# Kernel tuning notes

Measured on AMD Instinct MI355X. Metric: run time of the kernel, lower is better.

Reference implementation:

```python
import jax, jax.numpy as jnp
import numpy as np

DIM = 768
HEADS = 12
DIM_HEAD = DIM // HEADS
FACTOR = DIM_HEAD ** (-0.5)
B, T = 4, 2048


def setup_inputs() -> dict:
    key = jax.random.key(0)
    k1, k2, k3 = jax.random.split(key, 3)
    x = jax.random.normal(k1, (B, T, DIM), dtype=jnp.float32)
    # VarianceScaling-like init scale for linear weights
    W_qkv = jax.random.normal(k2, (DIM, 3 * DIM), dtype=jnp.float32) * (DIM ** -0.5)
    W_out = jax.random.normal(k3, (DIM, DIM), dtype=jnp.float32) * (DIM ** -0.5)
    return {"x": x, "W_qkv": W_qkv, "W_out": W_out}


def reference(x, W_qkv, W_out):
    b, t, _ = x.shape
    qkv = x @ W_qkv  # [b, t, 3*dim]
    # einops 'b t (d k h) -> k b h t d' with k=3, h=HEADS: d slowest, k middle, h fastest
    qkv = qkv.reshape(b, t, DIM_HEAD, 3, HEADS)
    qkv = jnp.transpose(qkv, (3, 0, 4, 1, 2))  # [3, b, h, t, d]
    q, k, v = qkv[0], qkv[1], qkv[2]
    # scaled dot-product attention, full [b,h,t,t] scores as in the original
    scores = jnp.einsum('bhid,bhjd->bhij', q, k) * FACTOR
    attn = jax.nn.softmax(scores, axis=-1)
    out = jnp.einsum('bhij,bhjd->bhid', attn, v)  # [b, h, t, d]
    # 'b h t d -> b t (h d)'
    out = jnp.transpose(out, (0, 2, 1, 3)).reshape(b, t, HEADS * DIM_HEAD)
    return out @ W_out
```

## Files before the change

kernel.cpp:

```cpp
#include <hip/hip_runtime.h>
#include <hip/hip_bf16.h>

#define DIM    768
#define HEADS  12
#define DHEAD  64
#define BATCH  4
#define SEQ    2048
#define NROW   (BATCH * SEQ)
#define QKVN   (3 * DIM)
#define FACTOR 0.125f
#define QSCALE 0.18033688011112042f

typedef __attribute__((ext_vector_type(8))) short short8;
typedef __attribute__((ext_vector_type(4))) float floatx4;

__device__ __forceinline__ floatx4 mfma16(short8 a, short8 b, floatx4 c) {
    return __builtin_amdgcn_mfma_f32_16x16x32_bf16(a, b, c, 0, 0, 0);
}

__device__ __forceinline__ void glds16(const void* g, void* l) {
    __builtin_amdgcn_global_load_lds((const __attribute__((address_space(1))) void*)g,
                                     (__attribute__((address_space(3))) void*)l,
                                     16, 0, 0);
}

__device__ __forceinline__ short rne16(float f) {
    unsigned u = __builtin_bit_cast(unsigned, f);
    return (short)((u + 0x7fffu + ((u >> 16) & 1u)) >> 16);
}
__device__ __forceinline__ unsigned pack2(float lo, float hi) {
    unsigned ul = __builtin_bit_cast(unsigned, lo);
    unsigned uh = __builtin_bit_cast(unsigned, hi);
    ul = (ul + 0x7fffu + ((ul >> 16) & 1u)) >> 16;
    uh = (uh + 0x7fffu + ((uh >> 16) & 1u)) & 0xffff0000u;
    return ul | uh;
}

__device__ __forceinline__ int swz8(int row, int col) {
    return (row << 6) + ((((col >> 3) ^ row) & 7) << 3) + (col & 7);
}

__global__ __launch_bounds__(256) void prep(const float* __restrict__ x,
                                            short* __restrict__ xb,
                                            const float* __restrict__ Wqkv,
                                            short* __restrict__ Wqt,
                                            const float* __restrict__ Wout,
                                            short* __restrict__ Wot) {
    __shared__ short T[32][33];
    int blk = blockIdx.x;
    if (blk < 6144) {
        int g = blk * 256 + threadIdx.x;
        float4 v = ((const float4*)x)[g];
        uint2 o;
        o.x = pack2(v.x, v.y);
        o.y = pack2(v.z, v.w);
        ((uint2*)xb)[g] = o;
        return;
    }
    blk -= 6144;
    const float* W;
    short* Wt;
    int N, permute, bx, by;
    if (blk < 1728) { W = Wqkv; Wt = Wqt; N = QKVN; permute = 1; bx = blk % 72; by = blk / 72; }
    else { blk -= 1728; W = Wout; Wt = Wot; N = DIM; permute = 0; bx = blk % 24; by = blk / 24; }

    int n0 = bx * 32, k0 = by * 32;
    int c = threadIdx.x & 31, r0 = threadIdx.x >> 5;
    for (int r = r0; r < 32; r += 8)
        T[r][c] = rne16(W[(size_t)(k0 + r) * N + n0 + c]);
    __syncthreads();
    for (int r = r0; r < 32; r += 8) {
        int n = n0 + r;
        int np = n;
        float scale = 1.0f;
        if (permute) {
            int d = n / 36, rem = n - d * 36;
            int which = rem / 12, h = rem - which * 12;
            np = which * 768 + h * 64 + d;
            if (which == 0) scale = QSCALE;
        }
        float v = __bfloat162float(__hip_bfloat16_raw{(unsigned short)T[c][r]});
        Wt[(size_t)np * DIM + k0 + c] = (scale == 1.0f) ? T[c][r] : rne16(v * scale);
    }
}

__global__ __launch_bounds__(256) void gemm_qkv(const short* __restrict__ A,
                                                const short* __restrict__ Bt,
                                                short* __restrict__ Qo,
                                                short* __restrict__ Ko,
                                                short* __restrict__ Vto) {
    __shared__ short As[128 * 64];
    __shared__ short Bs[128 * 64];
    const int tid = threadIdx.x;
    const int lane = tid & 63, wave = tid >> 6;
    const int l15 = lane & 15, quad = lane >> 4;

    const int flat = blockIdx.x;
    const int xcd = flat & 7;
    const int local = flat >> 3;
    const int mloc = local & 7, nloc = local >> 3;
    const int m0 = (xcd * 8 + mloc) * 128;
    const int n0 = nloc * 128;

    const int wm = (wave >> 1) * 64, wn = (wave & 1) * 64;
    const int r8 = wave * 8 + (lane >> 3);
    const int c8 = lane & 7;
    const int sc = ((c8 ^ (r8 & 7)) << 3);

    const int sn = n0 + wn;
    const int which = sn / 768;
    const bool swapAB = (which != 2);

    floatx4 acc[4][4] = {};
    for (int k0 = 0; k0 < DIM; k0 += 64) {
#pragma unroll
        for (int i = 0; i < 4; ++i) {
            int row = i * 32 + r8;
            glds16(&A[(size_t)(m0 + row) * DIM + k0 + sc], &As[(size_t)(i * 32 + wave * 8) * 64]);
            glds16(&Bt[(size_t)(n0 + row) * DIM + k0 + sc], &Bs[(size_t)(i * 32 + wave * 8) * 64]);
        }
        __syncthreads();
#pragma unroll
        for (int ks = 0; ks < 2; ++ks) {
            short8 a[4], b[4];
#pragma unroll
            for (int mt = 0; mt < 4; ++mt)
                a[mt] = *(const short8*)&As[swz8(wm + mt * 16 + l15, ks * 32 + quad * 8)];
#pragma unroll
            for (int nt = 0; nt < 4; ++nt)
                b[nt] = *(const short8*)&Bs[swz8(wn + nt * 16 + l15, ks * 32 + quad * 8)];
            if (swapAB) {
#pragma unroll
                for (int mt = 0; mt < 4; ++mt)
#pragma unroll
                    for (int nt = 0; nt < 4; ++nt)
                        acc[mt][nt] = mfma16(b[nt], a[mt], acc[mt][nt]);
            } else {
#pragma unroll
                for (int mt = 0; mt < 4; ++mt)
#pragma unroll
                    for (int nt = 0; nt < 4; ++nt)
                        acc[mt][nt] = mfma16(a[mt], b[nt], acc[mt][nt]);
            }
        }
        __syncthreads();
    }

    const int h = (sn - which * 768) >> 6;
    const int bb = (m0 + wm) >> 11;
    const int tbase = (m0 + wm) & 2047;
    const size_t tilebase = ((size_t)(bb * HEADS + h) * 32 + (tbase >> 6)) * 4096;

    if (which != 2) {
        short* dst = (which == 0) ? Qo : Ko;
#pragma unroll
        for (int mt = 0; mt < 4; ++mt)
#pragma unroll
            for (int nt = 0; nt < 4; ++nt) {
                int tl = mt * 16 + l15;
                int d0 = nt * 16 + quad * 4;
                uint2 pk;
                pk.x = pack2(acc[mt][nt][0], acc[mt][nt][1]);
                pk.y = pack2(acc[mt][nt][2], acc[mt][nt][3]);
                *(uint2*)&dst[tilebase + swz8(tl, d0)] = pk;
            }
    } else {
        short* vld = ((wave < 2) ? As : Bs) + (wave & 1) * 4096;
#pragma unroll
        for (int mt = 0; mt < 4; ++mt)
#pragma unroll
            for (int nt = 0; nt < 4; ++nt) {
                int d = nt * 16 + l15;
                int tl = mt * 16 + quad * 4;
                int chunk = (tl >> 3) ^ (d & 7);
                int addr = (d << 6) + (chunk << 3) + (tl & 7);
                uint2 pk;
                pk.x = pack2(acc[mt][nt][0], acc[mt][nt][1]);
                pk.y = pack2(acc[mt][nt][2], acc[mt][nt][3]);
                *(uint2*)&vld[addr] = pk;
            }
    }
    __syncthreads();
    if (which == 2) {
        short* vld = ((wave < 2) ? As : Bs) + (wave & 1) * 4096;
#pragma unroll
        for (int i = 0; i < 8; ++i) {
            int c = (i * 64 + lane) * 8;
            *(uint4*)&Vto[tilebase + c] = *(const uint4*)&vld[c];
        }
    }
}

__global__ __launch_bounds__(512, 6) void attn_mfma(const short* __restrict__ Q,
                                                    const short* __restrict__ K,
                                                    const short* __restrict__ Vt,
                                                    short* __restrict__ O) {
    __shared__ __align__(16) short buf[8192];
    __shared__ __align__(16) short Ps[8192];
    __shared__ float Lx[256];

    const int tid = threadIdx.x;
    const int lane = tid & 63, wave = tid >> 6;
    const int l15 = lane & 15, quad = lane >> 4;
    const int pair = wave >> 1, sh = wave & 1;
    const int flat = blockIdx.x;
    const int xcd = flat & 7, li = flat >> 3;
    const int bh = xcd + (li % 6) * 8;
    const int q0 = (li / 6) * 128;
    const size_t base = (size_t)bh * SEQ * DHEAD;
    short* Ks = buf;
    short* Vs = buf + 4096;
    short* Pp = Ps + pair * 2048;
    const int lane8 = lane * 8;

    {
        size_t qtb = base + (size_t)(q0 >> 6) * 4096;
#pragma unroll
        for (int i = 0; i < 2; ++i)
            glds16(&Q[qtb + (size_t)(i * 8 + wave) * 512 + lane8],
                   &buf[(i * 8 + wave) * 512]);
    }
    __syncthreads();
    short8 qf[2][2];
#pragma unroll
    for (int mt = 0; mt < 2; ++mt)
#pragma unroll
        for (int ks = 0; ks < 2; ++ks)
            qf[mt][ks] = *(const short8*)&buf[swz8(pair * 32 + mt * 16 + l15,
                                                   ks * 32 + quad * 8)];
    __syncthreads();

    floatx4 o[2][2] = {};
    float lsum[2] = {0.f, 0.f};

    for (int j0 = 0; j0 < SEQ; j0 += 64) {
        size_t ktb = base + (size_t)(j0 >> 6) * 4096 + wave * 512 + lane8;
        glds16(&K[ktb], &Ks[wave * 512]);
        glds16(&Vt[ktb], &Vs[wave * 512]);
        __syncthreads();

        floatx4 sa[2][2] = {};
#pragma unroll
        for (int ks = 0; ks < 2; ++ks) {
            short8 kf0 = *(const short8*)&Ks[swz8(sh * 32 + l15, ks * 32 + quad * 8)];
            short8 kf1 = *(const short8*)&Ks[swz8(sh * 32 + 16 + l15, ks * 32 + quad * 8)];
            sa[0][0] = mfma16(kf0, qf[0][ks], sa[0][0]);
            sa[0][1] = mfma16(kf1, qf[0][ks], sa[0][1]);
            sa[1][0] = mfma16(kf0, qf[1][ks], sa[1][0]);
            sa[1][1] = mfma16(kf1, qf[1][ks], sa[1][1]);
        }

#pragma unroll
        for (int mt = 0; mt < 2; ++mt)
#pragma unroll
            for (int kt = 0; kt < 2; ++kt) {
                float p0 = __builtin_amdgcn_exp2f(sa[mt][kt][0]);
                float p1 = __builtin_amdgcn_exp2f(sa[mt][kt][1]);
                float p2 = __builtin_amdgcn_exp2f(sa[mt][kt][2]);
                float p3 = __builtin_amdgcn_exp2f(sa[mt][kt][3]);
                lsum[mt] += (p0 + p1) + (p2 + p3);
                uint2 pk;
                pk.x = pack2(p0, p1);
                pk.y = pack2(p2, p3);
                *(uint2*)&Pp[swz8(mt * 16 + l15, sh * 32 + kt * 16 + quad * 4)] = pk;
            }
        __syncthreads();

#pragma unroll
        for (int ks = 0; ks < 2; ++ks) {
            short8 a0 = *(const short8*)&Pp[swz8(l15, ks * 32 + quad * 8)];
            short8 a1 = *(const short8*)&Pp[swz8(16 + l15, ks * 32 + quad * 8)];
            short8 b0 = *(const short8*)&Vs[swz8(sh * 32 + l15, ks * 32 + quad * 8)];
            short8 b1 = *(const short8*)&Vs[swz8(sh * 32 + 16 + l15, ks * 32 + quad * 8)];
            o[0][0] = mfma16(a0, b0, o[0][0]);
            o[0][1] = mfma16(a0, b1, o[0][1]);
            o[1][0] = mfma16(a1, b0, o[1][0]);
            o[1][1] = mfma16(a1, b1, o[1][1]);
        }
        __syncthreads();
    }

    float r0 = lsum[0], r1 = lsum[1];
    r0 += __shfl_xor(r0, 16); r0 += __shfl_xor(r0, 32);
    r1 += __shfl_xor(r1, 16); r1 += __shfl_xor(r1, 32);
    if (quad == 0) {
        Lx[pair * 64 + sh * 32 + l15] = r0;
        Lx[pair * 64 + sh * 32 + 16 + l15] = r1;
    }
    __syncthreads();
    float inv0 = 1.f / (r0 + Lx[pair * 64 + (sh ^ 1) * 32 + l15]);
    float inv1 = 1.f / (r1 + Lx[pair * 64 + (sh ^ 1) * 32 + 16 + l15]);

    const int b = bh / HEADS, h = bh - b * HEADS;
#pragma unroll
    for (int r = 0; r < 4; ++r) {
        float iv0 = __shfl(inv0, quad * 4 + r);
        float iv1 = __shfl(inv1, quad * 4 + r);
#pragma unroll
        for (int mt = 0; mt < 2; ++mt) {
            int t = q0 + pair * 32 + mt * 16 + quad * 4 + r;
            float iv = mt ? iv1 : iv0;
            size_t rowo = ((size_t)(b * SEQ + t)) * DIM + h * DHEAD + sh * 32;
            O[rowo + l15] = rne16(o[mt][0][r] * iv);
            O[rowo + 16 + l15] = rne16(o[mt][1][r] * iv);
        }
    }
}

__global__ __launch_bounds__(256) void gemm_out(const short* __restrict__ A,
                                                const short* __restrict__ Bt,
                                                float* __restrict__ out) {
    __shared__ short As[128 * 64];
    __shared__ short Bs[128 * 64];
    const int tid = threadIdx.x;
    const int lane = tid & 63, wave = tid >> 6;
    const int l15 = lane & 15, quad = lane >> 4;
    const int m0 = blockIdx.y * 128, n0 = blockIdx.x * 128;
    const int wm = (wave >> 1) * 64, wn = (wave & 1) * 64;
    const int r8 = wave * 8 + (lane >> 3);
    const int sc = (((lane & 7) ^ (r8 & 7)) << 3);

    floatx4 acc[4][4] = {};
    for (int k0 = 0; k0 < DIM; k0 += 64) {
#pragma unroll
        for (int i = 0; i < 4; ++i) {
            int row = i * 32 + r8;
            glds16(&A[(size_t)(m0 + row) * DIM + k0 + sc], &As[(size_t)(i * 32 + wave * 8) * 64]);
            glds16(&Bt[(size_t)(n0 + row) * DIM + k0 + sc], &Bs[(size_t)(i * 32 + wave * 8) * 64]);
        }
        __syncthreads();
#pragma unroll
        for (int ks = 0; ks < 2; ++ks) {
            short8 a[4], b[4];
#pragma unroll
            for (int mt = 0; mt < 4; ++mt)
                a[mt] = *(const short8*)&As[swz8(wm + mt * 16 + l15, ks * 32 + quad * 8)];
#pragma unroll
            for (int nt = 0; nt < 4; ++nt)
                b[nt] = *(const short8*)&Bs[swz8(wn + nt * 16 + l15, ks * 32 + quad * 8)];
#pragma unroll
            for (int mt = 0; mt < 4; ++mt)
#pragma unroll
                for (int nt = 0; nt < 4; ++nt)
                    acc[mt][nt] = mfma16(b[nt], a[mt], acc[mt][nt]);
        }
        __syncthreads();
    }

#pragma unroll
    for (int mt = 0; mt < 4; ++mt)
#pragma unroll
        for (int nt = 0; nt < 4; ++nt) {
            int m = m0 + wm + mt * 16 + l15;
            int n = n0 + wn + nt * 16 + quad * 4;
            *(floatx4*)&out[(size_t)m * DIM + n] = acc[mt][nt];
        }
}

extern "C" void kernel_launch(void* const* d_in, const int* in_sizes, int n_in,
                              void* d_out, int out_size, void* d_ws, size_t ws_size,
                              hipStream_t stream) {
    const float* x    = (const float*)d_in[0];
    const float* Wqkv = (const float*)d_in[1];
    const float* Wout = (const float*)d_in[2];
    float* out = (float*)d_out;

    const size_t NE = (size_t)NROW * DIM;
    short* xb  = (short*)d_ws;
    short* Wqt = xb + NE;
    short* Wot = Wqt + (size_t)QKVN * DIM;
    short* Qw  = Wot + (size_t)DIM * DIM;
    short* Kw  = Qw + NE;
    short* Vtw = Kw + NE;

    prep<<<6144 + 1728 + 576, 256, 0, stream>>>(x, xb, Wqkv, Wqt, Wout, Wot);
    gemm_qkv<<<8 * 8 * 18, 256, 0, stream>>>(xb, Wqt, Qw, Kw, Vtw);
    attn_mfma<<<768, 512, 0, stream>>>(Qw, Kw, Vtw, xb);
    gemm_out<<<dim3(DIM / 128, NROW / 128), 256, 0, stream>>>(xb, Wot, out);
}
```

Measured before the change: 218.1 us.

## Restructure attention kernel: one wave per query strip, double-buffered K/V

Rewrites the attention kernel so each of four waves owns 32 full query rows across all 64 keys and head dims. Wave pairs no longer split the work, which removes the per-tile P sync and the cross-wave row-sum exchange. K/V tiles are double-buffered in LDS, so the next tile loads while the current one is computed, and each iteration needs only one barrier. The change also uses the hardware bf16 pack instruction, s_setprio around MFMA blocks, and vectorized output stores. The costs are more registers per wave (larger accumulators), fewer threads per block, and more LDS for the second buffer.

Measured after the change: 213.5 us. 2.1% less time.

```diff
diff --git a/kernel.cpp b/kernel.cpp
--- a/kernel.cpp
+++ b/kernel.cpp
@@ -34,6 +34,11 @@
     ul = (ul + 0x7fffu + ((ul >> 16) & 1u)) >> 16;
     uh = (uh + 0x7fffu + ((uh >> 16) & 1u)) & 0xffff0000u;
     return ul | uh;
+}
+__device__ __forceinline__ unsigned cvtpk(float lo, float hi) {
+    unsigned r;
+    asm("v_cvt_pk_bf16_f32 %0, %1, %2" : "=v"(r) : "v"(lo), "v"(hi));
+    return r;
 }
 
 __device__ __forceinline__ int swz8(int row, int col) {
@@ -191,34 +196,29 @@
     }
 }
 
-__global__ __launch_bounds__(512, 6) void attn_mfma(const short* __restrict__ Q,
+__global__ __launch_bounds__(256, 3) void attn_mfma(const short* __restrict__ Q,
                                                     const short* __restrict__ K,
                                                     const short* __restrict__ Vt,
                                                     short* __restrict__ O) {
-    __shared__ __align__(16) short buf[8192];
-    __shared__ __align__(16) short Ps[8192];
-    __shared__ float Lx[256];
-
+    __shared__ __align__(16) short smem[24576];
     const int tid = threadIdx.x;
     const int lane = tid & 63, wave = tid >> 6;
     const int l15 = lane & 15, quad = lane >> 4;
-    const int pair = wave >> 1, sh = wave & 1;
     const int flat = blockIdx.x;
     const int xcd = flat & 7, li = flat >> 3;
     const int bh = xcd + (li % 6) * 8;
     const int q0 = (li / 6) * 128;
     const size_t base = (size_t)bh * SEQ * DHEAD;
-    short* Ks = buf;
-    short* Vs = buf + 4096;
-    short* Pp = Ps + pair * 2048;
+    short* Pp = smem + 16384 + wave * 2048;
     const int lane8 = lane * 8;
 
     {
         size_t qtb = base + (size_t)(q0 >> 6) * 4096;
 #pragma unroll
-        for (int i = 0; i < 2; ++i)
-            glds16(&Q[qtb + (size_t)(i * 8 + wave) * 512 + lane8],
-                   &buf[(i * 8 + wave) * 512]);
+        for (int c = 0; c < 4; ++c) {
+            int i = wave * 4 + c;
+            glds16(&Q[qtb + (size_t)i * 512 + lane8], &smem[i * 512]);
+        }
     }
     __syncthreads();
     short8 qf[2][2];
@@ -226,83 +226,98 @@
     for (int mt = 0; mt < 2; ++mt)
 #pragma unroll
         for (int ks = 0; ks < 2; ++ks)
-            qf[mt][ks] = *(const short8*)&buf[swz8(pair * 32 + mt * 16 + l15,
-                                                   ks * 32 + quad * 8)];
+            qf[mt][ks] = *(const short8*)&smem[(wave >> 1) * 4096 +
+                                               swz8((wave & 1) * 32 + mt * 16 + l15,
+                                                    ks * 32 + quad * 8)];
     __syncthreads();
 
-    floatx4 o[2][2] = {};
+    floatx4 o[4][2] = {};
     float lsum[2] = {0.f, 0.f};
 
-    for (int j0 = 0; j0 < SEQ; j0 += 64) {
-        size_t ktb = base + (size_t)(j0 >> 6) * 4096 + wave * 512 + lane8;
-        glds16(&K[ktb], &Ks[wave * 512]);
-        glds16(&Vt[ktb], &Vs[wave * 512]);
-        __syncthreads();
-
-        floatx4 sa[2][2] = {};
-#pragma unroll
-        for (int ks = 0; ks < 2; ++ks) {
-            short8 kf0 = *(const short8*)&Ks[swz8(sh * 32 + l15, ks * 32 + quad * 8)];
-            short8 kf1 = *(const short8*)&Ks[swz8(sh * 32 + 16 + l15, ks * 32 + quad * 8)];
-            sa[0][0] = mfma16(kf0, qf[0][ks], sa[0][0]);
-            sa[0][1] = mfma16(kf1, qf[0][ks], sa[0][1]);
-            sa[1][0] = mfma16(kf0, qf[1][ks], sa[1][0]);
-            sa[1][1] = mfma16(kf1, qf[1][ks], sa[1][1]);
-        }
-
-#pragma unroll
-        for (int mt = 0; mt < 2; ++mt)
-#pragma unroll
-            for (int kt = 0; kt < 2; ++kt) {
-                float p0 = __builtin_amdgcn_exp2f(sa[mt][kt][0]);
-                float p1 = __builtin_amdgcn_exp2f(sa[mt][kt][1]);
-                float p2 = __builtin_amdgcn_exp2f(sa[mt][kt][2]);
-                float p3 = __builtin_amdgcn_exp2f(sa[mt][kt][3]);
+    {
+#pragma unroll
+        for (int c = 0; c < 2; ++c) {
+            int i = wave * 2 + c;
+            glds16(&K[base + i * 512 + lane8], &smem[i * 512]);
+            glds16(&Vt[base + i * 512 + lane8], &smem[4096 + i * 512]);
+        }
+    }
+
+    for (int t = 0; t < 32; ++t) {
+        __syncthreads();
+        short* Ks = smem + (t & 1) * 8192;
+        short* Vs = Ks + 4096;
+        if (t < 31) {
+            size_t ktb = base + (size_t)(t + 1) * 4096;
+            short* nb = smem + ((t + 1) & 1) * 8192;
+#pragma unroll
+            for (int c = 0; c < 2; ++c) {
+                int i = wave * 2 + c;
+                glds16(&K[ktb + i * 512 + lane8], &nb[i * 512]);
+                glds16(&Vt[ktb + i * 512 + lane8], &nb[4096 + i * 512]);
+            }
+        }
+
+        floatx4 sa[4][2] = {};
+        __builtin_amdgcn_s_setprio(1);
+#pragma unroll
+        for (int ks = 0; ks < 2; ++ks)
+#pragma unroll
+            for (int kt = 0; kt < 4; ++kt) {
+                short8 kf = *(const short8*)&Ks[swz8(kt * 16 + l15, ks * 32 + quad * 8)];
+                sa[kt][0] = mfma16(kf, qf[0][ks], sa[kt][0]);
+                sa[kt][1] = mfma16(kf, qf[1][ks], sa[kt][1]);
+            }
+        __builtin_amdgcn_s_setprio(0);
+
+#pragma unroll
+        for (int kt = 0; kt < 4; ++kt)
+#pragma unroll
+            for (int mt = 0; mt < 2; ++mt) {
+                float p0 = __builtin_amdgcn_exp2f(sa[kt][mt][0]);
+                float p1 = __builtin_amdgcn_exp2f(sa[kt][mt][1]);
+                float p2 = __builtin_amdgcn_exp2f(sa[kt][mt][2]);
+                float p3 = __builtin_amdgcn_exp2f(sa[kt][mt][3]);
                 lsum[mt] += (p0 + p1) + (p2 + p3);
                 uint2 pk;
-                pk.x = pack2(p0, p1);
-                pk.y = pack2(p2, p3);
-                *(uint2*)&Pp[swz8(mt * 16 + l15, sh * 32 + kt * 16 + quad * 4)] = pk;
-            }
-        __syncthreads();
+                pk.x = cvtpk(p0, p1);
+                pk.y = cvtpk(p2, p3);
+                *(uint2*)&Pp[swz8(mt * 16 + l15, kt * 16 + quad * 4)] = pk;
+            }
 
 #pragma unroll
         for (int ks = 0; ks < 2; ++ks) {
-            short8 a0 = *(const short8*)&Pp[swz8(l15, ks * 32 + quad * 8)];
-            short8 a1 = *(const short8*)&Pp[swz8(16 + l15, ks * 32 + quad * 8)];
-            short8 b0 = *(const short8*)&Vs[swz8(sh * 32 + l15, ks * 32 + quad * 8)];
-            short8 b1 = *(const short8*)&Vs[swz8(sh * 32 + 16 + l15, ks * 32 + quad * 8)];
-            o[0][0] = mfma16(a0, b0, o[0][0]);
-            o[0][1] = mfma16(a0, b1, o[0][1]);
-            o[1][0] = mfma16(a1, b0, o[1][0]);
-            o[1][1] = mfma16(a1, b1, o[1][1]);
-        }
-        __syncthreads();
-    }
-
-    float r0 = lsum[0], r1 = lsum[1];
-    r0 += __shfl_xor(r0, 16); r0 += __shfl_xor(r0, 32);
-    r1 += __shfl_xor(r1, 16); r1 += __shfl_xor(r1, 32);
-    if (quad == 0) {
-        Lx[pair * 64 + sh * 32 + l15] = r0;
-        Lx[pair * 64 + sh * 32 + 16 + l15] = r1;
-    }
-    __syncthreads();
-    float inv0 = 1.f / (r0 + Lx[pair * 64 + (sh ^ 1) * 32 + l15]);
-    float inv1 = 1.f / (r1 + Lx[pair * 64 + (sh ^ 1) * 32 + 16 + l15]);
+            short8 pf0 = *(const short8*)&Pp[swz8(l15, ks * 32 + quad * 8)];
+            short8 pf1 = *(const short8*)&Pp[swz8(16 + l15, ks * 32 + quad * 8)];
+            __builtin_amdgcn_s_setprio(1);
+#pragma unroll
+            for (int dt = 0; dt < 4; ++dt) {
+                short8 vf = *(const short8*)&Vs[swz8(dt * 16 + l15, ks * 32 + quad * 8)];
+                o[dt][0] = mfma16(vf, pf0, o[dt][0]);
+                o[dt][1] = mfma16(vf, pf1, o[dt][1]);
+            }
+            __builtin_amdgcn_s_setprio(0);
+        }
+    }
+
+    float s0 = lsum[0], s1 = lsum[1];
+    s0 += __shfl_xor(s0, 16); s0 += __shfl_xor(s0, 32);
+    s1 += __shfl_xor(s1, 16); s1 += __shfl_xor(s1, 32);
+    float inv0 = 1.f / s0;
+    float inv1 = 1.f / s1;
 
     const int b = bh / HEADS, h = bh - b * HEADS;
 #pragma unroll
-    for (int r = 0; r < 4; ++r) {
-        float iv0 = __shfl(inv0, quad * 4 + r);
-        float iv1 = __shfl(inv1, quad * 4 + r);
-#pragma unroll
-        for (int mt = 0; mt < 2; ++mt) {
-            int t = q0 + pair * 32 + mt * 16 + quad * 4 + r;
-            float iv = mt ? iv1 : iv0;
-            size_t rowo = ((size_t)(b * SEQ + t)) * DIM + h * DHEAD + sh * 32;
-            O[rowo + l15] = rne16(o[mt][0][r] * iv);
-            O[rowo + 16 + l15] = rne16(o[mt][1][r] * iv);
+    for (int mt = 0; mt < 2; ++mt) {
+        int tq = q0 + wave * 32 + mt * 16 + l15;
+        float iv = mt ? inv1 : inv0;
+        size_t rowo = ((size_t)(b * SEQ + tq)) * DIM + h * DHEAD + quad * 4;
+#pragma unroll
+        for (int dt = 0; dt < 4; ++dt) {
+            uint2 pk;
+            pk.x = cvtpk(o[dt][mt][0] * iv, o[dt][mt][1] * iv);
+            pk.y = cvtpk(o[dt][mt][2] * iv, o[dt][mt][3] * iv);
+            *(uint2*)&O[rowo + dt * 16] = pk;
         }
     }
 }
@@ -375,6 +390,6 @@
 
     prep<<<6144 + 1728 + 576, 256, 0, stream>>>(x, xb, Wqkv, Wqt, Wout, Wot);
     gemm_qkv<<<8 * 8 * 18, 256, 0, stream>>>(xb, Wqt, Qw, Kw, Vtw);
-    attn_mfma<<<768, 512, 0, stream>>>(Qw, Kw, Vtw, xb);
+    attn_mfma<<<768, 256, 0, stream>>>(Qw, Kw, Vtw, xb);
     gemm_out<<<dim3(DIM / 128, NROW / 128), 256, 0, stream>>>(xb, Wot, out);
 }
```
